# Optimization experiments

Hardware: AMD Instinct MI355X
Metric: run time of the kernel (lower is better)

Reference implementation:

```python
import jax, jax.numpy as jnp
import numpy as np

N_SAMPLES = 8_000_000
N_TRAIN = 1_000_000
KS = 9
HALF_KS = (KS - 1) // 2  # 4
SIGMA = 1.0


def _build_stats():
    """Replicates LDSLoss.__init__: histogramdd, gaussian LDS smoothing, scaling."""
    rng = np.random.default_rng(0)
    labels = rng.uniform(0.0, 10.0, size=(N_TRAIN, 2))
    n_bins = int((labels.max() - labels.min()) / 0.1)
    hist, edges = np.histogramdd(labels, bins=n_bins)
    # gaussian_filter1d(impulse, sigma)/max == exp(-0.5*(x/sigma)^2), truncated at 4*sigma (= half_ks)
    x = np.arange(-HALF_KS, HALF_KS + 1, dtype=np.float64)
    kernel = np.exp(-0.5 * (x / SIGMA) ** 2)
    # scipy.ndimage.convolve1d(hist, kernel, mode='constant') acts along the LAST axis only;
    # kernel is symmetric so convolution == correlation.
    pad = np.pad(hist, ((0, 0), (HALF_KS, HALF_KS)))
    smoothed = np.zeros_like(hist)
    for k in range(KS):
        smoothed += kernel[k] * pad[:, k:k + n_bins]
    bins0 = edges[0]
    bins1 = edges[1]
    # scaling = len(w)/sum(w) with w = 1/smoothed[bin(label)] over the training labels
    i0 = np.clip(np.searchsorted(bins0, labels[:, 0], side='right') - 1, 0, n_bins - 1)
    i1 = np.clip(np.searchsorted(bins1, labels[:, 1], side='right') - 1, 0, n_bins - 1)
    w = 1.0 / smoothed[i0, i1]
    scaling = len(w) / w.sum()
    lo = np.array([bins0[0], bins1[0]])
    hi = np.array([bins0[-1], bins1[-1]])
    return (smoothed.astype(np.float32), bins0.astype(np.float32),
            bins1.astype(np.float32), np.float32(scaling), lo, hi)


def setup_inputs() -> dict:
    smoothed, bins0, bins1, scaling, lo, hi = _build_stats()
    key = jax.random.key(0)
    k1, k2 = jax.random.split(key)
    inp = jax.random.normal(k1, (N_SAMPLES, 2), dtype=jnp.float32)
    # targets drawn inside the training-label range (as histogram bins cover it)
    tgt = jax.random.uniform(k2, (N_SAMPLES, 2), dtype=jnp.float32,
                             minval=jnp.asarray(lo, jnp.float32),
                             maxval=jnp.asarray(hi, jnp.float32))
    return {
        "input": inp,
        "target": tgt,
        "smoothed_distribution": jnp.asarray(smoothed),
        "bins0": jnp.asarray(bins0),
        "bins1": jnp.asarray(bins1),
        "scaling": jnp.asarray(scaling),
    }


def reference(input, target, smoothed_distribution, bins0, bins1, scaling):
    nb = smoothed_distribution.shape[0]
    # torch.where(label < bins)[0][0] - 1  ==  searchsorted(bins, label, 'right') - 1,
    # with the 'no edge greater' case mapped to the last bin (len(bins)-2).
    i0 = jnp.clip(jnp.searchsorted(bins0, target[:, 0], side='right') - 1, 0, nb - 1)
    i1 = jnp.clip(jnp.searchsorted(bins1, target[:, 1], side='right') - 1, 0, nb - 1)
    kernel_weights = smoothed_distribution[i0, i1]          # irregular gather  [N]
    weights = 1.0 / kernel_weights
    inf_mask = jnp.isinf(weights)
    finite_max = jnp.max(jnp.where(inf_mask, -jnp.inf, weights))
    weights = jnp.where(inf_mask, finite_max, weights) * scaling
    loss = (input - target) ** 2                             # MSELoss(reduction='none')
    loss = loss * weights[:, None]
    return jnp.mean(loss)
```

## Files before the change

kernel.cpp:

```cpp
#include <hip/hip_runtime.h>
#include <math.h>


#define BLOCK 512
#define GRID_TARGET 1024

__device__ __forceinline__ int find_bin(const float* __restrict__ sb, int nb,
                                        float x, float lo, float inv_step) {
    int g = (int)floorf((x - lo) * inv_step);
    g = g < 0 ? 0 : (g > nb - 1 ? nb - 1 : g);
    #pragma unroll
    for (int s = 0; s < 2; ++s) {
        g -= (x < sb[g]) ? 1 : 0;
        g = g < 0 ? 0 : g;
        g += (x >= sb[g + 1]) ? 1 : 0;
        g = g > nb - 1 ? nb - 1 : g;
    }
    return g;
}

__device__ __forceinline__ void process_pair(
    float4 in, float4 tg,
    const float* __restrict__ sb0, const float* __restrict__ sb1,
    const float* __restrict__ stab, int nb,
    float lo0, float inv0, float lo1, float inv1,
    double& a, double& b, float& m)
{
    float dA0 = in.x - tg.x, dA1 = in.y - tg.y;
    float sqA = dA0 * dA0 + dA1 * dA1;
    int iA0 = find_bin(sb0, nb, tg.x, lo0, inv0);
    int iA1 = find_bin(sb1, nb, tg.y, lo1, inv1);
    float sA = stab[iA0 * nb + iA1];
    float dB0 = in.z - tg.z, dB1 = in.w - tg.w;
    float sqB = dB0 * dB0 + dB1 * dB1;
    int iB0 = find_bin(sb0, nb, tg.z, lo0, inv0);
    int iB1 = find_bin(sb1, nb, tg.w, lo1, inv1);
    float sB = stab[iB0 * nb + iB1];

    float wA = 1.0f / sA;
    if (isinf(wA)) { b += (double)sqA; }
    else           { a += (double)(wA * sqA); m = fmaxf(m, wA); }
    float wB = 1.0f / sB;
    if (isinf(wB)) { b += (double)sqB; }
    else           { a += (double)(wB * sqB); m = fmaxf(m, wB); }
}

__global__ void __launch_bounds__(BLOCK)
lds_loss_fused(const float* __restrict__ input,
               const float* __restrict__ target,
               const float* __restrict__ smoothed,
               const float* __restrict__ bins0,
               const float* __restrict__ bins1,
               const float* __restrict__ scaling,
               int nb, long long n, long long nelem,
               double* __restrict__ accA,
               double* __restrict__ accB,
               unsigned int* __restrict__ accM,
               unsigned int* __restrict__ done_ctr,
               float* __restrict__ out)
{
    extern __shared__ float smem[];
    float* sb0  = smem;
    float* sb1  = smem + (nb + 1);
    float* stab = smem + 2 * (nb + 1);

    for (int i = threadIdx.x; i < nb * nb; i += BLOCK) stab[i] = smoothed[i];
    for (int i = threadIdx.x; i < nb + 1; i += BLOCK) {
        sb0[i] = bins0[i];
        sb1[i] = bins1[i];
    }
    __syncthreads();

    const float lo0 = sb0[0], inv0 = (float)nb / (sb0[nb] - sb0[0]);
    const float lo1 = sb1[0], inv1 = (float)nb / (sb1[nb] - sb1[0]);

    double a = 0.0, b = 0.0;
    float  m = 0.0f;

    const long long npair = n >> 1;
    const float4* in4 = (const float4*)input;
    const float4* tg4 = (const float4*)target;
    const long long stride = (long long)gridDim.x * BLOCK;

    long long p = (long long)blockIdx.x * BLOCK + threadIdx.x;
    for (; p + 3 * stride < npair; p += 4 * stride) {
        float4 i0 = in4[p];
        float4 i1 = in4[p + stride];
        float4 i2 = in4[p + 2 * stride];
        float4 i3 = in4[p + 3 * stride];
        float4 t0 = tg4[p];
        float4 t1 = tg4[p + stride];
        float4 t2 = tg4[p + 2 * stride];
        float4 t3 = tg4[p + 3 * stride];
        process_pair(i0, t0, sb0, sb1, stab, nb, lo0, inv0, lo1, inv1, a, b, m);
        process_pair(i1, t1, sb0, sb1, stab, nb, lo0, inv0, lo1, inv1, a, b, m);
        process_pair(i2, t2, sb0, sb1, stab, nb, lo0, inv0, lo1, inv1, a, b, m);
        process_pair(i3, t3, sb0, sb1, stab, nb, lo0, inv0, lo1, inv1, a, b, m);
    }
    for (; p < npair; p += stride) {
        process_pair(in4[p], tg4[p], sb0, sb1, stab, nb,
                     lo0, inv0, lo1, inv1, a, b, m);
    }

    if ((n & 1) && blockIdx.x == 0 && threadIdx.x == 0) {
        long long i = n - 1;
        float t0 = target[2 * i], t1 = target[2 * i + 1];
        float d0 = input[2 * i] - t0, d1 = input[2 * i + 1] - t1;
        float sq = d0 * d0 + d1 * d1;
        int j0 = find_bin(sb0, nb, t0, lo0, inv0);
        int j1 = find_bin(sb1, nb, t1, lo1, inv1);
        float w = 1.0f / stab[j0 * nb + j1];
        if (isinf(w)) { b += (double)sq; }
        else          { a += (double)(w * sq); m = fmaxf(m, w); }
    }

    #pragma unroll
    for (int off = 32; off > 0; off >>= 1) {
        a += __shfl_down(a, off, 64);
        b += __shfl_down(b, off, 64);
        m = fmaxf(m, __shfl_down(m, off, 64));
    }

    __shared__ double sA[BLOCK / 64], sB[BLOCK / 64];
    __shared__ float  sM[BLOCK / 64];
    int wave = threadIdx.x >> 6;
    int lane = threadIdx.x & 63;
    if (lane == 0) { sA[wave] = a; sB[wave] = b; sM[wave] = m; }
    __syncthreads();

    if (threadIdx.x == 0) {
        double ta = 0.0, tb = 0.0; float tm = 0.0f;
        #pragma unroll
        for (int w2 = 0; w2 < BLOCK / 64; ++w2) {
            ta += sA[w2]; tb += sB[w2]; tm = fmaxf(tm, sM[w2]);
        }
        atomicAdd(accA, ta);
        atomicAdd(accB, tb);
        atomicMax(accM, __float_as_uint(tm));
        __threadfence();
        unsigned int prev = atomicAdd(done_ctr, 1u);
        if (prev == gridDim.x - 1) {
            double A = atomicAdd(accA, 0.0);
            double B = atomicAdd(accB, 0.0);
            float  M = __uint_as_float(atomicMax(accM, 0u));
            double v = (double)(*scaling) * (A + (double)M * B) / (double)nelem;
            *out = (float)v;
        }
    }
}

extern "C" void kernel_launch(void* const* d_in, const int* in_sizes, int n_in,
                              void* d_out, int out_size, void* d_ws, size_t ws_size,
                              hipStream_t stream) {
    const float* input    = (const float*)d_in[0];
    const float* target   = (const float*)d_in[1];
    const float* smoothed = (const float*)d_in[2];
    const float* bins0    = (const float*)d_in[3];
    const float* bins1    = (const float*)d_in[4];
    const float* scaling  = (const float*)d_in[5];

    const long long nelem = in_sizes[0];
    const long long n     = nelem / 2;
    const int nb          = in_sizes[3] - 1;

    double*       accA = (double*)d_ws;
    double*       accB = accA + 1;
    unsigned int* accM = (unsigned int*)(accB + 1);
    unsigned int* ctr  = accM + 1;

    hipMemsetAsync(d_ws, 0, 24, stream);

    long long blocks_needed = (n / 2 + BLOCK - 1) / BLOCK;
    int grid = (int)(blocks_needed < GRID_TARGET ? blocks_needed : GRID_TARGET);
    if (grid < 1) grid = 1;
    size_t shmem = ((size_t)2 * (nb + 1) + (size_t)nb * nb) * sizeof(float);

    lds_loss_fused<<<grid, BLOCK, shmem, stream>>>(
        input, target, smoothed, bins0, bins1, scaling,
        nb, n, nelem, accA, accB, accM, ctr, (float*)d_out);
}
```

Measured before the change: 200.1 us.

## Accumulate per-bin squared errors in shared histogram, apply weights once per bin

Each block now keeps a shared-memory histogram of squared errors per 2D bin, filled with LDS float atomics. Weights (1/smoothed) and the finite-max and inf handling are applied once per bin at the end, not per sample. This removes the per-sample division, branch and double-precision accumulation. The bin search is cut to a single correction step, and the atomic counter plus memset finalisation is replaced by a cooperative launch with a grid-wide sync. The risks are shared-atomic contention, an extra per-block pass over all bins, a smaller grid, and float rather than double accumulation inside each bin.

```diff
diff --git a/kernel.cpp b/kernel.cpp
--- a/kernel.cpp
+++ b/kernel.cpp
@@ -1,70 +1,63 @@
 #include <hip/hip_runtime.h>
+#include <hip/hip_cooperative_groups.h>
 #include <math.h>
 
+namespace cg = cooperative_groups;
+
 
 #define BLOCK 512
-#define GRID_TARGET 1024
+#define GRID_BLKS 512
 
 __device__ __forceinline__ int find_bin(const float* __restrict__ sb, int nb,
                                         float x, float lo, float inv_step) {
     int g = (int)floorf((x - lo) * inv_step);
     g = g < 0 ? 0 : (g > nb - 1 ? nb - 1 : g);
-    #pragma unroll
-    for (int s = 0; s < 2; ++s) {
-        g -= (x < sb[g]) ? 1 : 0;
-        g = g < 0 ? 0 : g;
-        g += (x >= sb[g + 1]) ? 1 : 0;
-        g = g > nb - 1 ? nb - 1 : g;
-    }
-    return g;
+    float e0 = sb[g];
+    float e1 = sb[g + 1];
+    g += (x >= e1) ? 1 : 0;
+    g -= (x < e0) ? 1 : 0;
+    return g < 0 ? 0 : (g > nb - 1 ? nb - 1 : g);
 }
 
 __device__ __forceinline__ void process_pair(
     float4 in, float4 tg,
-    const float* __restrict__ sb0, const float* __restrict__ sb1,
-    const float* __restrict__ stab, int nb,
-    float lo0, float inv0, float lo1, float inv1,
-    double& a, double& b, float& m)
+    float* __restrict__ hist,
+    const float* __restrict__ sb0, const float* __restrict__ sb1, int nb,
+    float lo0, float inv0, float lo1, float inv1)
 {
     float dA0 = in.x - tg.x, dA1 = in.y - tg.y;
     float sqA = dA0 * dA0 + dA1 * dA1;
     int iA0 = find_bin(sb0, nb, tg.x, lo0, inv0);
     int iA1 = find_bin(sb1, nb, tg.y, lo1, inv1);
-    float sA = stab[iA0 * nb + iA1];
+    atomicAdd(&hist[iA0 * nb + iA1], sqA);
+
     float dB0 = in.z - tg.z, dB1 = in.w - tg.w;
     float sqB = dB0 * dB0 + dB1 * dB1;
     int iB0 = find_bin(sb0, nb, tg.z, lo0, inv0);
     int iB1 = find_bin(sb1, nb, tg.w, lo1, inv1);
-    float sB = stab[iB0 * nb + iB1];
-
-    float wA = 1.0f / sA;
-    if (isinf(wA)) { b += (double)sqA; }
-    else           { a += (double)(wA * sqA); m = fmaxf(m, wA); }
-    float wB = 1.0f / sB;
-    if (isinf(wB)) { b += (double)sqB; }
-    else           { a += (double)(wB * sqB); m = fmaxf(m, wB); }
+    atomicAdd(&hist[iB0 * nb + iB1], sqB);
 }
 
 __global__ void __launch_bounds__(BLOCK)
-lds_loss_fused(const float* __restrict__ input,
-               const float* __restrict__ target,
-               const float* __restrict__ smoothed,
-               const float* __restrict__ bins0,
-               const float* __restrict__ bins1,
-               const float* __restrict__ scaling,
-               int nb, long long n, long long nelem,
-               double* __restrict__ accA,
-               double* __restrict__ accB,
-               unsigned int* __restrict__ accM,
-               unsigned int* __restrict__ done_ctr,
-               float* __restrict__ out)
+lds_loss_coop(const float* __restrict__ input,
+              const float* __restrict__ target,
+              const float* __restrict__ smoothed,
+              const float* __restrict__ bins0,
+              const float* __restrict__ bins1,
+              const float* __restrict__ scaling,
+              int nb, long long n, long long nelem,
+              double* __restrict__ partA,
+              double* __restrict__ partB,
+              float* __restrict__ partM,
+              float* __restrict__ out)
 {
-    extern __shared__ float smem[];
-    float* sb0  = smem;
-    float* sb1  = smem + (nb + 1);
-    float* stab = smem + 2 * (nb + 1);
-
-    for (int i = threadIdx.x; i < nb * nb; i += BLOCK) stab[i] = smoothed[i];
+    extern __shared__ __align__(16) float smem[];
+    float* hist = smem;
+    float* sb0  = smem + nb * nb;
+    float* sb1  = sb0 + (nb + 1);
+
+    const int nbnb = nb * nb;
+    for (int i = threadIdx.x; i < nbnb; i += BLOCK) hist[i] = 0.0f;
     for (int i = threadIdx.x; i < nb + 1; i += BLOCK) {
         sb0[i] = bins0[i];
         sb1[i] = bins1[i];
@@ -73,9 +66,6 @@
 
     const float lo0 = sb0[0], inv0 = (float)nb / (sb0[nb] - sb0[0]);
     const float lo1 = sb1[0], inv1 = (float)nb / (sb1[nb] - sb1[0]);
-
-    double a = 0.0, b = 0.0;
-    float  m = 0.0f;
 
     const long long npair = n >> 1;
     const float4* in4 = (const float4*)input;
@@ -92,14 +82,13 @@
         float4 t1 = tg4[p + stride];
         float4 t2 = tg4[p + 2 * stride];
         float4 t3 = tg4[p + 3 * stride];
-        process_pair(i0, t0, sb0, sb1, stab, nb, lo0, inv0, lo1, inv1, a, b, m);
-        process_pair(i1, t1, sb0, sb1, stab, nb, lo0, inv0, lo1, inv1, a, b, m);
-        process_pair(i2, t2, sb0, sb1, stab, nb, lo0, inv0, lo1, inv1, a, b, m);
-        process_pair(i3, t3, sb0, sb1, stab, nb, lo0, inv0, lo1, inv1, a, b, m);
+        process_pair(i0, t0, hist, sb0, sb1, nb, lo0, inv0, lo1, inv1);
+        process_pair(i1, t1, hist, sb0, sb1, nb, lo0, inv0, lo1, inv1);
+        process_pair(i2, t2, hist, sb0, sb1, nb, lo0, inv0, lo1, inv1);
+        process_pair(i3, t3, hist, sb0, sb1, nb, lo0, inv0, lo1, inv1);
     }
     for (; p < npair; p += stride) {
-        process_pair(in4[p], tg4[p], sb0, sb1, stab, nb,
-                     lo0, inv0, lo1, inv1, a, b, m);
+        process_pair(in4[p], tg4[p], hist, sb0, sb1, nb, lo0, inv0, lo1, inv1);
     }
 
     if ((n & 1) && blockIdx.x == 0 && threadIdx.x == 0) {
@@ -109,41 +98,73 @@
         float sq = d0 * d0 + d1 * d1;
         int j0 = find_bin(sb0, nb, t0, lo0, inv0);
         int j1 = find_bin(sb1, nb, t1, lo1, inv1);
-        float w = 1.0f / stab[j0 * nb + j1];
-        if (isinf(w)) { b += (double)sq; }
-        else          { a += (double)(w * sq); m = fmaxf(m, w); }
+        atomicAdd(&hist[j0 * nb + j1], sq);
+    }
+    __syncthreads();
+
+    double A = 0.0, B = 0.0;
+    float  m = 0.0f;
+    for (int b = threadIdx.x; b < nbnb; b += BLOCK) {
+        float h = hist[b];
+        float s = smoothed[b];
+        if (s == 0.0f) {
+            B += (double)h;
+        } else {
+            float w = 1.0f / s;
+            A += (double)w * (double)h;
+            if (h > 0.0f) m = fmaxf(m, w);
+        }
     }
 
     #pragma unroll
     for (int off = 32; off > 0; off >>= 1) {
-        a += __shfl_down(a, off, 64);
-        b += __shfl_down(b, off, 64);
+        A += __shfl_down(A, off, 64);
+        B += __shfl_down(B, off, 64);
         m = fmaxf(m, __shfl_down(m, off, 64));
     }
 
-    __shared__ double sA[BLOCK / 64], sB[BLOCK / 64];
-    __shared__ float  sM[BLOCK / 64];
+    __syncthreads();
+    double* rA = (double*)smem;
+    double* rB = rA + (BLOCK / 64);
+    float*  rM = (float*)(rB + (BLOCK / 64));
     int wave = threadIdx.x >> 6;
     int lane = threadIdx.x & 63;
-    if (lane == 0) { sA[wave] = a; sB[wave] = b; sM[wave] = m; }
-    __syncthreads();
-
+    if (lane == 0) { rA[wave] = A; rB[wave] = B; rM[wave] = m; }
+    __syncthreads();
     if (threadIdx.x == 0) {
         double ta = 0.0, tb = 0.0; float tm = 0.0f;
         #pragma unroll
         for (int w2 = 0; w2 < BLOCK / 64; ++w2) {
-            ta += sA[w2]; tb += sB[w2]; tm = fmaxf(tm, sM[w2]);
-        }
-        atomicAdd(accA, ta);
-        atomicAdd(accB, tb);
-        atomicMax(accM, __float_as_uint(tm));
-        __threadfence();
-        unsigned int prev = atomicAdd(done_ctr, 1u);
-        if (prev == gridDim.x - 1) {
-            double A = atomicAdd(accA, 0.0);
-            double B = atomicAdd(accB, 0.0);
-            float  M = __uint_as_float(atomicMax(accM, 0u));
-            double v = (double)(*scaling) * (A + (double)M * B) / (double)nelem;
+            ta += rA[w2]; tb += rB[w2]; tm = fmaxf(tm, rM[w2]);
+        }
+        partA[blockIdx.x] = ta;
+        partB[blockIdx.x] = tb;
+        partM[blockIdx.x] = tm;
+    }
+
+    cg::this_grid().sync();
+
+    if (blockIdx.x == 0) {
+        int t = threadIdx.x;
+        double a2 = (t < (int)gridDim.x) ? partA[t] : 0.0;
+        double b2 = (t < (int)gridDim.x) ? partB[t] : 0.0;
+        float  m2 = (t < (int)gridDim.x) ? partM[t] : 0.0f;
+        #pragma unroll
+        for (int off = 32; off > 0; off >>= 1) {
+            a2 += __shfl_down(a2, off, 64);
+            b2 += __shfl_down(b2, off, 64);
+            m2 = fmaxf(m2, __shfl_down(m2, off, 64));
+        }
+        __syncthreads();
+        if (lane == 0) { rA[wave] = a2; rB[wave] = b2; rM[wave] = m2; }
+        __syncthreads();
+        if (t == 0) {
+            double ta = 0.0, tb = 0.0; float tm = 0.0f;
+            #pragma unroll
+            for (int w2 = 0; w2 < BLOCK / 64; ++w2) {
+                ta += rA[w2]; tb += rB[w2]; tm = fmaxf(tm, rM[w2]);
+            }
+            double v = (double)(*scaling) * (ta + (double)tm * tb) / (double)nelem;
             *out = (float)v;
         }
     }
@@ -159,23 +180,26 @@
     const float* bins1    = (const float*)d_in[4];
     const float* scaling  = (const float*)d_in[5];
 
-    const long long nelem = in_sizes[0];
-    const long long n     = nelem / 2;
-    const int nb          = in_sizes[3] - 1;
-
-    double*       accA = (double*)d_ws;
-    double*       accB = accA + 1;
-    unsigned int* accM = (unsigned int*)(accB + 1);
-    unsigned int* ctr  = accM + 1;
-
-    hipMemsetAsync(d_ws, 0, 24, stream);
-
-    long long blocks_needed = (n / 2 + BLOCK - 1) / BLOCK;
-    int grid = (int)(blocks_needed < GRID_TARGET ? blocks_needed : GRID_TARGET);
-    if (grid < 1) grid = 1;
-    size_t shmem = ((size_t)2 * (nb + 1) + (size_t)nb * nb) * sizeof(float);
-
-    lds_loss_fused<<<grid, BLOCK, shmem, stream>>>(
-        input, target, smoothed, bins0, bins1, scaling,
-        nb, n, nelem, accA, accB, accM, ctr, (float*)d_out);
-}
+    long long nelem = in_sizes[0];
+    long long n     = nelem / 2;
+    int       nb    = in_sizes[3] - 1;
+
+    double* partA = (double*)d_ws;
+    double* partB = partA + GRID_BLKS;
+    float*  partM = (float*)(partB + GRID_BLKS);
+    float*  out   = (float*)d_out;
+
+    unsigned int shmem =
+        (unsigned int)(((size_t)nb * nb + 2 * (nb + 1)) * sizeof(float));
+
+    void* args[] = {
+        (void*)&input, (void*)&target, (void*)&smoothed,
+        (void*)&bins0, (void*)&bins1, (void*)&scaling,
+        (void*)&nb, (void*)&n, (void*)&nelem,
+        (void*)&partA, (void*)&partB, (void*)&partM, (void*)&out
+    };
+
+    hipLaunchCooperativeKernel((void*)lds_loss_coop,
+                               dim3(GRID_BLKS), dim3(BLOCK),
+                               args, shmem, stream);
+}
```

After: 234.2 us. 1.17x slower.
